# Performance work log

Hardware: AMD Instinct MI355X
Metric: run time of the kernel (lower is better)

The kernel has to match this reference:

```python
import jax, jax.numpy as jnp
import numpy as np

H = 16  # num_heads

def _split_heads(x, h):
    B, T, D = x.shape
    return x.reshape(B, T, h, D // h).transpose(0, 2, 1, 3)  # [B,h,T,d]

def setup_inputs() -> dict:
    key = jax.random.key(0)
    ks = jax.random.split(key, 7)
    B, T, D = 2, 2048, 2048
    s = 0.02
    return {
        "x": jax.random.normal(ks[0], (B, T, D), dtype=jnp.float32),
        "Wq1": jax.random.normal(ks[1], (D, D), dtype=jnp.float32) * s,
        "Wq2": jax.random.normal(ks[2], (D, D), dtype=jnp.float32) * s,
        "Wk": jax.random.normal(ks[3], (D, D), dtype=jnp.float32) * s,
        "Wv": jax.random.normal(ks[4], (D, D), dtype=jnp.float32) * s,
        "Wlam": jax.random.normal(ks[5], (D, H), dtype=jnp.float32) * s,
        "Wo": jax.random.normal(ks[6], (D, D), dtype=jnp.float32) * s,
    }

def reference(x, Wq1, Wq2, Wk, Wv, Wlam, Wo):
    B, T, D = x.shape
    d = D // H
    q1 = _split_heads(x @ Wq1, H)
    q2 = _split_heads(x @ Wq2, H)
    k = _split_heads(x @ Wk, H)
    v = _split_heads(x @ Wv, H)
    q = jnp.concatenate([q1, q2], axis=1)        # [B,2H,T,d] (q1 heads then q2 heads)
    k2 = jnp.repeat(k, 2, axis=1)                # [B,2H,T,d] (adjacent duplication, as torch repeat_interleave)
    v2 = jnp.repeat(v, 2, axis=1)
    scale = 1.0 / jnp.sqrt(jnp.asarray(d, dtype=x.dtype))
    scores = jnp.einsum("bhqd,bhkd->bhqk", q, k2) * scale
    causal = jnp.tril(jnp.ones((T, T), dtype=bool))
    scores = jnp.where(causal, scores, jnp.finfo(scores.dtype).min)
    p = jax.nn.softmax(scores, axis=-1)
    y = jnp.einsum("bhqk,bhkd->bhqd", p, v2)     # [B,2H,T,d]
    y1, y2 = y[:, :H], y[:, H:]
    lam = jax.nn.sigmoid(x @ Wlam).transpose(0, 2, 1)[..., None]  # [B,H,T,1]
    y = y1 - lam * y2                            # [B,H,T,d]
    y = y.transpose(0, 2, 1, 3).reshape(B, T, D)
    return y @ Wo
```

## Files before the change

### kernel.cpp

```cpp
#include <hip/hip_runtime.h>
#include <stdint.h>

#define Bb 2
#define Tt 2048
#define Dd 2048
#define Hh 16
#define HD 128
#define NTOK (Bb*Tt)

typedef _Float16 f16;
typedef unsigned short u16;
typedef __attribute__((ext_vector_type(8))) _Float16 f16x8;
typedef __attribute__((ext_vector_type(4))) _Float16 f16x4;
typedef __attribute__((ext_vector_type(4))) float f32x4;

__device__ __forceinline__ void gl2lds16(const f16* g, f16* l) {
  __builtin_amdgcn_global_load_lds(
      (const __attribute__((address_space(1))) unsigned int*)(const_cast<f16*>(g)),
      (__attribute__((address_space(3))) unsigned int*)(l),
      16, 0, 0);
}

__global__ void cvt_x_kernel(const float* __restrict__ x, f16* __restrict__ xh) {
  const int n4 = NTOK * Dd / 4;
  int i = blockIdx.x * 256 + threadIdx.x;
  const int stride = gridDim.x * 256;
  for (; i < n4; i += stride) {
    float4 v = ((const float4*)x)[i];
    f16x4 o;
    o.x = (f16)v.x; o.y = (f16)v.y; o.z = (f16)v.z; o.w = (f16)v.w;
    ((f16x4*)xh)[i] = o;
  }
}

__global__ void wtrans_kernel(const float* __restrict__ W0, const float* __restrict__ W1,
                              const float* __restrict__ W2, const float* __restrict__ W3,
                              const float* __restrict__ W4, f16* __restrict__ wt) {
  const float* W;
  int z = blockIdx.z;
  if (z == 0) W = W0; else if (z == 1) W = W1; else if (z == 2) W = W2;
  else if (z == 3) W = W3; else W = W4;
  f16* dst = wt + (size_t)z * Dd * Dd;
  __shared__ f16 tile[64][65];
  const int k0 = blockIdx.y * 64, n0 = blockIdx.x * 64;
  const int tr = threadIdx.x >> 6, tc = threadIdx.x & 63;
#pragma unroll
  for (int p = 0; p < 16; ++p) {
    int r = tr + p * 4;
    tile[r][tc] = (f16)W[(size_t)(k0 + r) * Dd + n0 + tc];
  }
  __syncthreads();
#pragma unroll
  for (int p = 0; p < 16; ++p) {
    int r = tr + p * 4;
    dst[(size_t)(n0 + r) * Dd + k0 + tc] = tile[tc][r];
  }
}

template <int OUTF16>
__global__ __launch_bounds__(256) void gemm_bt_kernel(
    const f16* __restrict__ A, const f16* __restrict__ Bt0,
    unsigned long long bt_stride, void* __restrict__ Cb, unsigned long long c_stride) {
  __shared__ __align__(16) f16 Alds[128 * 32];
  __shared__ __align__(16) f16 Blds[128 * 32];
  const f16* Bt = Bt0 + (size_t)blockIdx.z * bt_stride;
  const int m0 = blockIdx.y * 128, n0 = blockIdx.x * 128;
  const int tid = threadIdx.x, wid = tid >> 6, lane = tid & 63;
  const int quad = lane >> 4, l15 = lane & 15;
  const int srow = lane >> 2, sch = lane & 3;
  const int g = (l15 >> 1) & 3;
  const int koff = (quad ^ g) * 8;
  const int mw = (wid >> 1) * 64, nw = (wid & 1) * 64;
  const int sg = sch ^ ((srow >> 1) & 3);
  f32x4 acc[4][4] = {};
  for (int kk = 0; kk < Dd; kk += 32) {
#pragma unroll
    for (int j = 0; j < 2; ++j) {
      const int c = wid * 2 + j;
      const int row = c * 16 + srow;
      gl2lds16(A + (size_t)(m0 + row) * Dd + kk + sg * 8, &Alds[c * 512]);
      gl2lds16(Bt + (size_t)(n0 + row) * Dd + kk + sg * 8, &Blds[c * 512]);
    }
    __syncthreads();
    f16x8 af[4], bfr[4];
#pragma unroll
    for (int t = 0; t < 4; ++t)
      af[t] = *(const f16x8*)&Alds[(mw + t * 16 + l15) * 32 + koff];
#pragma unroll
    for (int t = 0; t < 4; ++t)
      bfr[t] = *(const f16x8*)&Blds[(nw + t * 16 + l15) * 32 + koff];
#pragma unroll
    for (int mt = 0; mt < 4; ++mt)
#pragma unroll
      for (int nt = 0; nt < 4; ++nt)
        acc[mt][nt] = __builtin_amdgcn_mfma_f32_16x16x32_f16(af[mt], bfr[nt], acc[mt][nt], 0, 0, 0);
    __syncthreads();
  }
  const size_t czoff = (size_t)blockIdx.z * c_stride;
#pragma unroll
  for (int mt = 0; mt < 4; ++mt) {
    const int r0 = m0 + mw + mt * 16 + quad * 4;
#pragma unroll
    for (int r = 0; r < 4; ++r) {
#pragma unroll
      for (int nt = 0; nt < 4; ++nt) {
        const int col = n0 + nw + nt * 16 + l15;
        const float v = acc[mt][nt][r];
        if (OUTF16)
          ((f16*)Cb)[czoff + (size_t)(r0 + r) * Dd + col] = (f16)v;
        else
          ((float*)Cb)[czoff + (size_t)(r0 + r) * Dd + col] = v;
      }
    }
  }
}

__global__ __launch_bounds__(256) void lam_kernel(const f16* __restrict__ xh,
                                                  const float* __restrict__ Wlam,
                                                  float* __restrict__ lamb) {
  const int wid = threadIdx.x >> 6, lane = threadIdx.x & 63;
  const int tok = blockIdx.x * 4 + wid;
  const f16* xr = xh + (size_t)tok * Dd;
  float acc[16] = {};
#pragma unroll
  for (int j = 0; j < 4; ++j) {
    const int k0 = j * 512 + lane * 8;
    f16x8 xv = *(const f16x8*)(xr + k0);
#pragma unroll
    for (int e = 0; e < 8; ++e) {
      const float xe = (float)xv[e];
      const float4* wr = (const float4*)(Wlam + (size_t)(k0 + e) * Hh);
#pragma unroll
      for (int q = 0; q < 4; ++q) {
        float4 w = wr[q];
        acc[q * 4 + 0] = fmaf(xe, w.x, acc[q * 4 + 0]);
        acc[q * 4 + 1] = fmaf(xe, w.y, acc[q * 4 + 1]);
        acc[q * 4 + 2] = fmaf(xe, w.z, acc[q * 4 + 2]);
        acc[q * 4 + 3] = fmaf(xe, w.w, acc[q * 4 + 3]);
      }
    }
  }
#pragma unroll
  for (int ofs = 32; ofs >= 1; ofs >>= 1)
#pragma unroll
    for (int i = 0; i < 16; ++i) acc[i] += __shfl_xor(acc[i], ofs);
  if (lane == 0) {
#pragma unroll
    for (int i = 0; i < 16; ++i)
      lamb[tok * Hh + i] = 1.f / (1.f + __expf(-acc[i]));
  }
}

__global__ void vtrans_kernel(const f16* __restrict__ vb, f16* __restrict__ vtb) {
  const int z = blockIdx.z;
  const int b = z >> 4, hv = z & 15;
  const int t0 = blockIdx.x * 64, d0 = blockIdx.y * 64;
  __shared__ f16 tile[64][65];
  const int tr = threadIdx.x >> 6, tc = threadIdx.x & 63;
#pragma unroll
  for (int p = 0; p < 16; ++p) {
    int r = tr + p * 4;
    tile[r][tc] = vb[(size_t)(b * Tt + t0 + r) * Dd + hv * HD + d0 + tc];
  }
  __syncthreads();
  const int u = tc & 31;
  const int tp = (tc & 32) | (((u >> 2) & 3) * 8 + ((u >> 4) & 1) * 4 + (u & 3));
#pragma unroll
  for (int p = 0; p < 16; ++p) {
    int r = tr + p * 4;
    vtb[((size_t)z * HD + d0 + r) * Tt + t0 + tp] = tile[tc][r];
  }
}

__global__ __launch_bounds__(256, 2) void attn_kernel(
    const f16* __restrict__ q1b, const f16* __restrict__ q2b,
    const f16* __restrict__ kbuf, const f16* __restrict__ vtb,
    f16* __restrict__ yah) {
  __shared__ __align__(16) f16 Klds[2][64 * 128];
  __shared__ __align__(16) f16 Vlds[2][128 * 64];
  const int bx = blockIdx.x;
  const int qt = (bx & 1) ? (15 - (bx >> 1)) : (bx >> 1);
  const int h = blockIdx.y, b = blockIdx.z;
  const int hkv = h >> 1;
  const f16* qb = (h < Hh) ? q1b : q2b;
  const int hq = h & 15;
  const int tid = threadIdx.x, wid = tid >> 6, lane = tid & 63;
  const int quad = lane >> 4, l15 = lane & 15;
  const int qbase = qt * 128 + wid * 32;
  const int ntiles = 2 * qt + 2;
  const f16 qscale = (f16)(0.08838834764831845f * 1.4426950408889634f);

  f16x8 qf0[4], qf1[4];
  {
    const f16* qp0 = qb + (size_t)(b * Tt + qbase + l15) * Dd + hq * HD + quad * 8;
    const f16* qp1 = qp0 + (size_t)16 * Dd;
#pragma unroll
    for (int ks = 0; ks < 4; ++ks) { qf0[ks] = *(const f16x8*)(qp0 + ks * 32); qf1[ks] = *(const f16x8*)(qp1 + ks * 32); }
#pragma unroll
    for (int ks = 0; ks < 4; ++ks) { qf0[ks] *= qscale; qf1[ks] *= qscale; }
  }

  uint32_t koffg[4], voffg[4];
#pragma unroll
  for (int p = 0; p < 4; ++p) {
    const int krow = wid * 16 + p * 4 + (lane >> 4);
    const int kch = (lane & 15) ^ (krow & 7);
    koffg[p] = (uint32_t)((b * Tt + krow) * Dd + hkv * HD + kch * 8);
    const int vrow = wid * 32 + p * 8 + (lane >> 3);
    const int vch = (lane & 7) ^ (vrow & 7);
    voffg[p] = (uint32_t)(((b * 16 + hkv) * HD + vrow) * Tt + vch * 8);
  }

  f32x4 o0[8] = {}, o1[8] = {};
  float m_0 = -3.0e38f, m_1 = -3.0e38f, l_0 = 0.f, l_1 = 0.f;

#define ISSUE_TILE(KT, PAR)                                                        \
  {                                                                                \
    const uint32_t kshift = (uint32_t)(KT) * 64 * Dd;                              \
    const uint32_t vshift = (uint32_t)(KT) * 64;                                   \
    _Pragma("unroll") for (int p = 0; p < 4; ++p)                                  \
        gl2lds16(kbuf + kshift + koffg[p], &Klds[PAR][(wid * 16 + p * 4) * 128]);  \
    _Pragma("unroll") for (int p = 0; p < 4; ++p)                                  \
        gl2lds16(vtb + vshift + voffg[p], &Vlds[PAR][(wid * 32 + p * 8) * 64]);    \
  }

  ISSUE_TILE(0, 0);
  ISSUE_TILE(1, 1);

  for (int kt = 0; kt < ntiles; ++kt) {
    const int cur = kt & 1;
    if (kt + 1 < ntiles) asm volatile("s_waitcnt vmcnt(8)\n\ts_barrier" ::: "memory");
    else                 asm volatile("s_waitcnt vmcnt(0)\n\ts_barrier" ::: "memory");

    if (kt * 64 <= qbase + 31) {
      const f16* Kl = &Klds[cur][0];
      const f16* Vl = &Vlds[cur][0];

      f32x4 s0[4] = {}, s1[4] = {};
#pragma unroll
      for (int nt = 0; nt < 4; ++nt) {
        const int r = nt * 16 + l15;
#pragma unroll
        for (int ks = 0; ks < 4; ++ks) {
          f16x8 kf = *(const f16x8*)&Kl[r * 128 + (((ks * 4 + quad) ^ (l15 & 7)) << 3)];
          s0[nt] = __builtin_amdgcn_mfma_f32_16x16x32_f16(kf, qf0[ks], s0[nt], 0, 0, 0);
          s1[nt] = __builtin_amdgcn_mfma_f32_16x16x32_f16(kf, qf1[ks], s1[nt], 0, 0, 0);
        }
      }
      if (kt * 64 + 63 > qbase) {
        const int q0 = qbase + l15, q1_ = q0 + 16;
#pragma unroll
        for (int nt = 0; nt < 4; ++nt) {
          const int keyb = kt * 64 + nt * 16 + quad * 4;
#pragma unroll
          for (int r = 0; r < 4; ++r) {
            if (keyb + r > q0) s0[nt][r] = -3.0e38f;
            if (keyb + r > q1_) s1[nt][r] = -3.0e38f;
          }
        }
      }
      float tm0 = s0[0][0], tm1 = s1[0][0];
#pragma unroll
      for (int nt = 0; nt < 4; ++nt)
#pragma unroll
        for (int r = 0; r < 4; ++r) { tm0 = fmaxf(tm0, s0[nt][r]); tm1 = fmaxf(tm1, s1[nt][r]); }
      tm0 = fmaxf(tm0, __shfl_xor(tm0, 16)); tm1 = fmaxf(tm1, __shfl_xor(tm1, 16));
      tm0 = fmaxf(tm0, __shfl_xor(tm0, 32)); tm1 = fmaxf(tm1, __shfl_xor(tm1, 32));
      const float mo0 = m_0, mo1 = m_1;
      m_0 = fmaxf(m_0, tm0); m_1 = fmaxf(m_1, tm1);
      float rs0 = 0.f, rs1 = 0.f;
      f16x4 pf0[4], pf1[4];
#pragma unroll
      for (int nt = 0; nt < 4; ++nt) {
        float a0 = exp2f(s0[nt][0] - m_0), a1 = exp2f(s0[nt][1] - m_0);
        float a2 = exp2f(s0[nt][2] - m_0), a3 = exp2f(s0[nt][3] - m_0);
        float b0 = exp2f(s1[nt][0] - m_1), b1 = exp2f(s1[nt][1] - m_1);
        float b2 = exp2f(s1[nt][2] - m_1), b3 = exp2f(s1[nt][3] - m_1);
        rs0 += (a0 + a1) + (a2 + a3);
        rs1 += (b0 + b1) + (b2 + b3);
        pf0[nt].x = (f16)a0; pf0[nt].y = (f16)a1; pf0[nt].z = (f16)a2; pf0[nt].w = (f16)a3;
        pf1[nt].x = (f16)b0; pf1[nt].y = (f16)b1; pf1[nt].z = (f16)b2; pf1[nt].w = (f16)b3;
      }
      rs0 += __shfl_xor(rs0, 16); rs1 += __shfl_xor(rs1, 16);
      rs0 += __shfl_xor(rs0, 32); rs1 += __shfl_xor(rs1, 32);
      if (__ballot((m_0 > mo0) | (m_1 > mo1))) {
        const float al0 = exp2f(mo0 - m_0), al1 = exp2f(mo1 - m_1);
        l_0 *= al0; l_1 *= al1;
        float ar0[4], ar1[4];
#pragma unroll
        for (int r = 0; r < 4; ++r) { ar0[r] = __shfl(al0, quad * 4 + r); ar1[r] = __shfl(al1, quad * 4 + r); }
#pragma unroll
        for (int n2 = 0; n2 < 8; ++n2)
#pragma unroll
          for (int r = 0; r < 4; ++r) { o0[n2][r] *= ar0[r]; o1[n2][r] *= ar1[r]; }
      }
      l_0 += rs0; l_1 += rs1;
#pragma unroll
      for (int g = 0; g < 2; ++g) {
#pragma unroll
        for (int n2 = 0; n2 < 8; ++n2) {
          const int d_ = n2 * 16 + l15;
          f16x8 vf = *(const f16x8*)&Vl[d_ * 64 + (((g * 4 + quad) ^ (l15 & 7)) << 3)];
          f16x4 vlo = __builtin_shufflevector(vf, vf, 0, 1, 2, 3);
          f16x4 vhi = __builtin_shufflevector(vf, vf, 4, 5, 6, 7);
          o0[n2] = __builtin_amdgcn_mfma_f32_16x16x16f16(pf0[2 * g], vlo, o0[n2], 0, 0, 0);
          o0[n2] = __builtin_amdgcn_mfma_f32_16x16x16f16(pf0[2 * g + 1], vhi, o0[n2], 0, 0, 0);
          o1[n2] = __builtin_amdgcn_mfma_f32_16x16x16f16(pf1[2 * g], vlo, o1[n2], 0, 0, 0);
          o1[n2] = __builtin_amdgcn_mfma_f32_16x16x16f16(pf1[2 * g + 1], vhi, o1[n2], 0, 0, 0);
        }
      }
    }
    asm volatile("s_waitcnt lgkmcnt(0)\n\ts_barrier" ::: "memory");
    if (kt + 2 < ntiles) ISSUE_TILE(kt + 2, cur);
  }
#undef ISSUE_TILE

  float lr0[4], lr1[4];
#pragma unroll
  for (int r = 0; r < 4; ++r) { lr0[r] = __shfl(l_0, quad * 4 + r); lr1[r] = __shfl(l_1, quad * 4 + r); }
#pragma unroll
  for (int r = 0; r < 4; ++r) {
    const float i0 = 1.0f / lr0[r], i1 = 1.0f / lr1[r];
    const int row0 = qbase + quad * 4 + r;
    f16* d0_ = yah + ((size_t)(b * 32 + h) * Tt + row0) * HD;
    f16* d1_ = d0_ + (size_t)16 * HD;
#pragma unroll
    for (int n2 = 0; n2 < 8; ++n2) {
      d0_[n2 * 16 + l15] = (f16)(o0[n2][r] * i0);
      d1_[n2 * 16 + l15] = (f16)(o1[n2][r] * i1);
    }
  }
}

__global__ void combine_kernel(const f16* __restrict__ yah, const float* __restrict__ lamb,
                               f16* __restrict__ ybf) {
  const int n4 = NTOK * Dd / 4;
  int i = blockIdx.x * 256 + threadIdx.x;
  const int stride = gridDim.x * 256;
  for (; i < n4; i += stride) {
    const int e0 = i * 4;
    const int dc = e0 & 127;
    const int hh = (e0 >> 7) & 15;
    const int tt = (e0 >> 11) & 2047;
    const int bb = e0 >> 22;
    const size_t base1 = ((size_t)(bb * 32 + hh) * Tt + tt) * HD + dc;
    const size_t base2 = ((size_t)(bb * 32 + 16 + hh) * Tt + tt) * HD + dc;
    f16x4 y1 = *(const f16x4*)(yah + base1);
    f16x4 y2 = *(const f16x4*)(yah + base2);
    const float lam = lamb[(bb * Tt + tt) * Hh + hh];
    f16x4 o;
    o.x = (f16)((float)y1.x - lam * (float)y2.x);
    o.y = (f16)((float)y1.y - lam * (float)y2.y);
    o.z = (f16)((float)y1.z - lam * (float)y2.z);
    o.w = (f16)((float)y1.w - lam * (float)y2.w);
    *(f16x4*)(ybf + e0) = o;
  }
}

extern "C" void kernel_launch(void* const* d_in, const int* in_sizes, int n_in,
                              void* d_out, int out_size, void* d_ws, size_t ws_size,
                              hipStream_t stream) {
  const float* x    = (const float*)d_in[0];
  const float* Wq1  = (const float*)d_in[1];
  const float* Wq2  = (const float*)d_in[2];
  const float* Wk   = (const float*)d_in[3];
  const float* Wv   = (const float*)d_in[4];
  const float* Wlam = (const float*)d_in[5];
  const float* Wo   = (const float*)d_in[6];

  f16* xbf = (f16*)d_ws;
  f16* wt  = xbf + (size_t)NTOK * Dd;
  f16* q1b = wt + 5ull * Dd * Dd;
  f16* q2b = q1b + (size_t)NTOK * Dd;
  f16* kbf = q2b + (size_t)NTOK * Dd;
  f16* vbf = kbf + (size_t)NTOK * Dd;
  f16* vtb = vbf + (size_t)NTOK * Dd;
  float* lamb = (float*)(vtb + (size_t)NTOK * Dd);
  f16* yah = (f16*)(lamb + (size_t)NTOK * Hh);
  f16* ybf = xbf;

  cvt_x_kernel<<<dim3(2048), dim3(256), 0, stream>>>(x, xbf);
  wtrans_kernel<<<dim3(32, 32, 5), dim3(256), 0, stream>>>(Wq1, Wq2, Wk, Wv, Wo, wt);
  gemm_bt_kernel<1><<<dim3(16, 32, 4), dim3(256), 0, stream>>>(
      xbf, wt, (unsigned long long)Dd * Dd, (void*)q1b, (unsigned long long)NTOK * Dd);
  lam_kernel<<<dim3(NTOK / 4), dim3(256), 0, stream>>>(xbf, Wlam, lamb);
  vtrans_kernel<<<dim3(32, 2, 32), dim3(256), 0, stream>>>(vbf, vtb);
  attn_kernel<<<dim3(16, 32, 2), dim3(256), 0, stream>>>(q1b, q2b, kbf, vtb, yah);
  combine_kernel<<<dim3(2048), dim3(256), 0, stream>>>(yah, lamb, ybf);
  gemm_bt_kernel<0><<<dim3(16, 32, 1), dim3(256), 0, stream>>>(
      ybf, wt + 4ull * Dd * Dd, 0ull, d_out, 0ull);
}
```

Baseline: 664.1 us.

## Fuse lambda projection into x conversion and restructure attention K/V buffering

Merges the fp16 conversion of x with the sigmoid-lambda projection into one kernel that reads fp32 x directly, dropping a launch and a re-read of the converted activations. In attention, the K tile becomes single-buffered and V stays double-buffered, with the next tile's loads issued after QK^T rather than two tiles ahead. The smaller LDS footprint allows launch bounds of 3 blocks per CU for more occupancy, at the cost of less prefetch distance and an extra full barrier per tile. The lambda path now uses fp32 x instead of the fp16-rounded values.

```diff
diff --git a/kernel.cpp b/kernel.cpp
--- a/kernel.cpp
+++ b/kernel.cpp
@@ -21,15 +21,45 @@
       16, 0, 0);
 }
 
-__global__ void cvt_x_kernel(const float* __restrict__ x, f16* __restrict__ xh) {
-  const int n4 = NTOK * Dd / 4;
-  int i = blockIdx.x * 256 + threadIdx.x;
-  const int stride = gridDim.x * 256;
-  for (; i < n4; i += stride) {
-    float4 v = ((const float4*)x)[i];
+__global__ __launch_bounds__(256) void cvtlam_kernel(const float* __restrict__ x,
+                                                     const float* __restrict__ Wlam,
+                                                     f16* __restrict__ xh,
+                                                     float* __restrict__ lamb) {
+  const int wid = threadIdx.x >> 6, lane = threadIdx.x & 63;
+  const int tok = blockIdx.x * 4 + wid;
+  const float* xr = x + (size_t)tok * Dd;
+  f16* xo = xh + (size_t)tok * Dd;
+  float acc[16] = {};
+#pragma unroll
+  for (int j = 0; j < 8; ++j) {
+    const int k0 = j * 256 + lane * 4;
+    float4 v = *(const float4*)(xr + k0);
     f16x4 o;
     o.x = (f16)v.x; o.y = (f16)v.y; o.z = (f16)v.z; o.w = (f16)v.w;
-    ((f16x4*)xh)[i] = o;
+    *(f16x4*)(xo + k0) = o;
+    const float xe4[4] = {v.x, v.y, v.z, v.w};
+#pragma unroll
+    for (int e = 0; e < 4; ++e) {
+      const float xe = xe4[e];
+      const float4* wr = (const float4*)(Wlam + (size_t)(k0 + e) * Hh);
+#pragma unroll
+      for (int q = 0; q < 4; ++q) {
+        float4 w = wr[q];
+        acc[q * 4 + 0] = fmaf(xe, w.x, acc[q * 4 + 0]);
+        acc[q * 4 + 1] = fmaf(xe, w.y, acc[q * 4 + 1]);
+        acc[q * 4 + 2] = fmaf(xe, w.z, acc[q * 4 + 2]);
+        acc[q * 4 + 3] = fmaf(xe, w.w, acc[q * 4 + 3]);
+      }
+    }
+  }
+#pragma unroll
+  for (int ofs = 32; ofs >= 1; ofs >>= 1)
+#pragma unroll
+    for (int i = 0; i < 16; ++i) acc[i] += __shfl_xor(acc[i], ofs);
+  if (lane == 0) {
+#pragma unroll
+    for (int i = 0; i < 16; ++i)
+      lamb[tok * Hh + i] = 1.f / (1.f + __expf(-acc[i]));
   }
 }
 
@@ -115,42 +145,6 @@
   }
 }
 
-__global__ __launch_bounds__(256) void lam_kernel(const f16* __restrict__ xh,
-                                                  const float* __restrict__ Wlam,
-                                                  float* __restrict__ lamb) {
-  const int wid = threadIdx.x >> 6, lane = threadIdx.x & 63;
-  const int tok = blockIdx.x * 4 + wid;
-  const f16* xr = xh + (size_t)tok * Dd;
-  float acc[16] = {};
-#pragma unroll
-  for (int j = 0; j < 4; ++j) {
-    const int k0 = j * 512 + lane * 8;
-    f16x8 xv = *(const f16x8*)(xr + k0);
-#pragma unroll
-    for (int e = 0; e < 8; ++e) {
-      const float xe = (float)xv[e];
-      const float4* wr = (const float4*)(Wlam + (size_t)(k0 + e) * Hh);
-#pragma unroll
-      for (int q = 0; q < 4; ++q) {
-        float4 w = wr[q];
-        acc[q * 4 + 0] = fmaf(xe, w.x, acc[q * 4 + 0]);
-        acc[q * 4 + 1] = fmaf(xe, w.y, acc[q * 4 + 1]);
-        acc[q * 4 + 2] = fmaf(xe, w.z, acc[q * 4 + 2]);
-        acc[q * 4 + 3] = fmaf(xe, w.w, acc[q * 4 + 3]);
-      }
-    }
-  }
-#pragma unroll
-  for (int ofs = 32; ofs >= 1; ofs >>= 1)
-#pragma unroll
-    for (int i = 0; i < 16; ++i) acc[i] += __shfl_xor(acc[i], ofs);
-  if (lane == 0) {
-#pragma unroll
-    for (int i = 0; i < 16; ++i)
-      lamb[tok * Hh + i] = 1.f / (1.f + __expf(-acc[i]));
-  }
-}
-
 __global__ void vtrans_kernel(const f16* __restrict__ vb, f16* __restrict__ vtb) {
   const int z = blockIdx.z;
   const int b = z >> 4, hv = z & 15;
@@ -172,11 +166,11 @@
   }
 }
 
-__global__ __launch_bounds__(256, 2) void attn_kernel(
+__global__ __launch_bounds__(256, 3) void attn_kernel(
     const f16* __restrict__ q1b, const f16* __restrict__ q2b,
     const f16* __restrict__ kbuf, const f16* __restrict__ vtb,
     f16* __restrict__ yah) {
-  __shared__ __align__(16) f16 Klds[2][64 * 128];
+  __shared__ __align__(16) f16 Klds[64 * 128];
   __shared__ __align__(16) f16 Vlds[2][128 * 64];
   const int bx = blockIdx.x;
   const int qt = (bx & 1) ? (15 - (bx >> 1)) : (bx >> 1);
@@ -214,39 +208,43 @@
   f32x4 o0[8] = {}, o1[8] = {};
   float m_0 = -3.0e38f, m_1 = -3.0e38f, l_0 = 0.f, l_1 = 0.f;
 
-#define ISSUE_TILE(KT, PAR)                                                        \
+#define ISSUE_K(KT)                                                                \
   {                                                                                \
     const uint32_t kshift = (uint32_t)(KT) * 64 * Dd;                              \
+    _Pragma("unroll") for (int p = 0; p < 4; ++p)                                  \
+        gl2lds16(kbuf + kshift + koffg[p], &Klds[(wid * 16 + p * 4) * 128]);       \
+  }
+#define ISSUE_V(KT)                                                                \
+  {                                                                                \
     const uint32_t vshift = (uint32_t)(KT) * 64;                                   \
+    f16* vb_ = &Vlds[(KT) & 1][0];                                                 \
     _Pragma("unroll") for (int p = 0; p < 4; ++p)                                  \
-        gl2lds16(kbuf + kshift + koffg[p], &Klds[PAR][(wid * 16 + p * 4) * 128]);  \
-    _Pragma("unroll") for (int p = 0; p < 4; ++p)                                  \
-        gl2lds16(vtb + vshift + voffg[p], &Vlds[PAR][(wid * 32 + p * 8) * 64]);    \
-  }
-
-  ISSUE_TILE(0, 0);
-  ISSUE_TILE(1, 1);
+        gl2lds16(vtb + vshift + voffg[p], &vb_[(wid * 32 + p * 8) * 64]);          \
+  }
+
+  ISSUE_K(0);
+  ISSUE_V(0);
 
   for (int kt = 0; kt < ntiles; ++kt) {
-    const int cur = kt & 1;
-    if (kt + 1 < ntiles) asm volatile("s_waitcnt vmcnt(8)\n\ts_barrier" ::: "memory");
-    else                 asm volatile("s_waitcnt vmcnt(0)\n\ts_barrier" ::: "memory");
-
-    if (kt * 64 <= qbase + 31) {
-      const f16* Kl = &Klds[cur][0];
-      const f16* Vl = &Vlds[cur][0];
-
-      f32x4 s0[4] = {}, s1[4] = {};
+    asm volatile("s_waitcnt vmcnt(4)\n\ts_barrier" ::: "memory");
+    const bool live = (kt * 64 <= qbase + 31);
+    f32x4 s0[4] = {}, s1[4] = {};
+    if (live) {
 #pragma unroll
       for (int nt = 0; nt < 4; ++nt) {
         const int r = nt * 16 + l15;
 #pragma unroll
         for (int ks = 0; ks < 4; ++ks) {
-          f16x8 kf = *(const f16x8*)&Kl[r * 128 + (((ks * 4 + quad) ^ (l15 & 7)) << 3)];
+          f16x8 kf = *(const f16x8*)&Klds[r * 128 + (((ks * 4 + quad) ^ (l15 & 7)) << 3)];
           s0[nt] = __builtin_amdgcn_mfma_f32_16x16x32_f16(kf, qf0[ks], s0[nt], 0, 0, 0);
           s1[nt] = __builtin_amdgcn_mfma_f32_16x16x32_f16(kf, qf1[ks], s1[nt], 0, 0, 0);
         }
       }
+    }
+    asm volatile("s_waitcnt vmcnt(0) lgkmcnt(0)\n\ts_barrier" ::: "memory");
+    if (kt + 1 < ntiles) { ISSUE_K(kt + 1); ISSUE_V(kt + 1); }
+    if (live) {
+      const f16* Vl = &Vlds[kt & 1][0];
       if (kt * 64 + 63 > qbase) {
         const int q0 = qbase + l15, q1_ = q0 + 16;
 #pragma unroll
@@ -310,10 +308,9 @@
         }
       }
     }
-    asm volatile("s_waitcnt lgkmcnt(0)\n\ts_barrier" ::: "memory");
-    if (kt + 2 < ntiles) ISSUE_TILE(kt + 2, cur);
-  }
-#undef ISSUE_TILE
+  }
+#undef ISSUE_K
+#undef ISSUE_V
 
   float lr0[4], lr1[4];
 #pragma unroll
@@ -379,11 +376,10 @@
   f16* yah = (f16*)(lamb + (size_t)NTOK * Hh);
   f16* ybf = xbf;
 
-  cvt_x_kernel<<<dim3(2048), dim3(256), 0, stream>>>(x, xbf);
+  cvtlam_kernel<<<dim3(NTOK / 4), dim3(256), 0, stream>>>(x, Wlam, xbf, lamb);
   wtrans_kernel<<<dim3(32, 32, 5), dim3(256), 0, stream>>>(Wq1, Wq2, Wk, Wv, Wo, wt);
   gemm_bt_kernel<1><<<dim3(16, 32, 4), dim3(256), 0, stream>>>(
       xbf, wt, (unsigned long long)Dd * Dd, (void*)q1b, (unsigned long long)NTOK * Dd);
-  lam_kernel<<<dim3(NTOK / 4), dim3(256), 0, stream>>>(xbf, Wlam, lamb);
   vtrans_kernel<<<dim3(32, 2, 32), dim3(256), 0, stream>>>(vbf, vtb);
   attn_kernel<<<dim3(16, 32, 2), dim3(256), 0, stream>>>(q1b, q2b, kbf, vtb, yah);
   combine_kernel<<<dim3(2048), dim3(256), 0, stream>>>(yah, lamb, ybf);
```

After: 774.9 us. 16.7% more time.
